# Kernel optimization log

Hardware: AMD Instinct MI355X
Metric: run time of the kernel (lower is better)

The kernel has to match this reference:

```python
import jax, jax.numpy as jnp
import numpy as np

RBF_CO = 10.077141124806595


def setup_inputs() -> dict:
    key = jax.random.key(0)
    k1, k2, k3 = jax.random.split(key, 3)
    n, dim = 2048, 128
    N, out_dim = 50000, 64
    features = jax.random.normal(k1, (n, dim), dtype=jnp.float32)
    train_data = jax.random.normal(k2, (N, dim), dtype=jnp.float32)
    weights = jax.random.normal(k3, (N, out_dim), dtype=jnp.float32) * 0.02
    return {"features": features, "train_data": train_data, "weights": weights}


def reference(features, train_data, weights):
    x2 = jnp.sum(features * features, axis=-1, keepdims=True)      # [n, 1]
    t2 = jnp.sum(train_data * train_data, axis=-1)                 # [N]
    d2 = x2 + t2[None, :] - 2.0 * (features @ train_data.T)        # [n, N]
    dist = jnp.sqrt(jnp.maximum(d2, 0.0))                          # clamp fp error
    k = jnp.exp(-dist / RBF_CO / 2.0)                              # RBF kernel [n, N]
    return k @ weights                                              # [n, out_dim]
```

## Files before the change

### kernel.cpp

```cpp
#include <hip/hip_runtime.h>
#include <hip/hip_bf16.h>
#include <stdint.h>

#define DIM 128
#define ODIM 64
#define BM 128
#define BN 64
#define NSPLIT 64

typedef __attribute__((ext_vector_type(8))) __bf16 bf16x8;
typedef __attribute__((ext_vector_type(4))) __bf16 bf16x4;
typedef __attribute__((ext_vector_type(2))) __bf16 bf16x2;
typedef __attribute__((ext_vector_type(4))) float f32x4;

#define MFMA_K32(a, b, c) __builtin_amdgcn_mfma_f32_16x16x32_bf16((a), (b), (c), 0, 0, 0)
#define MFMA_K16(a, b, c) __builtin_amdgcn_mfma_f32_16x16x16bf16_1k((a), (b), (c), 0, 0, 0)

#define RBFD 10.077141124806595
#define LOG2E 1.4426950408889634
#define C2D ((LOG2E / (2.0 * RBFD)) * (LOG2E / (2.0 * RBFD)))

__device__ __forceinline__ void async_copy16(const void* g, void* l) {
  __builtin_amdgcn_global_load_lds((const __attribute__((address_space(1))) void*)g,
                                   (__attribute__((address_space(3))) void*)l, 16, 0, 0);
}
__device__ __forceinline__ void async_copy4(const void* g, void* l) {
  __builtin_amdgcn_global_load_lds((const __attribute__((address_space(1))) void*)g,
                                   (__attribute__((address_space(3))) void*)l, 4, 0, 0);
}

__device__ __forceinline__ uint32_t pack_bf16(float a, float b) {
  uint32_t ua = __builtin_bit_cast(uint32_t, a) + 0x8000u;
  uint32_t ub = __builtin_bit_cast(uint32_t, b) + 0x8000u;
  return __builtin_amdgcn_perm(ub, ua, 0x07060302u);
}

__global__ void prep_all(const float* __restrict__ train, __bf16* __restrict__ Tb,
                         float* __restrict__ t2, const float* __restrict__ feat,
                         __bf16* __restrict__ Fb, float* __restrict__ x2,
                         const float* __restrict__ W, __bf16* __restrict__ Wt,
                         int Ntrain, int Npad, int nFeat, int tB, int fB, float scale) {
  __shared__ float tile[64][65];
  int b = blockIdx.x;
  int t = threadIdx.x;
  if (b < tB + fB) {
    const float* src;
    __bf16* dst;
    float* sq;
    int nValid, nPad, row0;
    float padv;
    if (b < tB) {
      src = train; dst = Tb; sq = t2; nValid = Ntrain; nPad = Npad; row0 = b * 4; padv = 1e30f;
    } else {
      src = feat; dst = Fb; sq = x2; nValid = nFeat; nPad = nFeat; row0 = (b - tB) * 4; padv = 0.0f;
    }
    int row = row0 + (t >> 6);
    int lane = t & 63;
    if (row >= nPad) return;
    float2 v = make_float2(0.0f, 0.0f);
    if (row < nValid) v = ((const float2*)src)[(size_t)row * 64 + lane];
    bf16x2 p;
    p.x = (__bf16)v.x;
    p.y = (__bf16)v.y;
    *(bf16x2*)&dst[(size_t)row * DIM + lane * 2] = p;
    float ss = v.x * v.x + v.y * v.y;
    #pragma unroll
    for (int off = 32; off > 0; off >>= 1) ss += __shfl_down(ss, off);
    if (lane == 0) sq[row] = (row < nValid) ? ss * scale : padv;
    return;
  }
  int j0 = (b - tB - fB) * 64;
  int jr = t >> 2;
  int cg = (t & 3) * 16;
  int j = j0 + jr;
  if (j < Ntrain) {
    const float4* src = (const float4*)(W + (size_t)j * ODIM);
    #pragma unroll
    for (int q = 0; q < 4; ++q) {
      float4 u = src[(cg >> 2) + q];
      tile[jr][cg + q * 4 + 0] = u.x;
      tile[jr][cg + q * 4 + 1] = u.y;
      tile[jr][cg + q * 4 + 2] = u.z;
      tile[jr][cg + q * 4 + 3] = u.w;
    }
  } else {
    #pragma unroll
    for (int q = 0; q < 16; ++q) tile[jr][cg + q] = 0.0f;
  }
  __syncthreads();
  int v = t >> 2;
  int jc = (t & 3) * 16;
  __bf16 ob[16];
  #pragma unroll
  for (int q = 0; q < 16; ++q) ob[q] = (__bf16)tile[jc + q][v];
  __bf16* dst = Wt + (size_t)v * Npad + j0 + jc;
  *(bf16x8*)dst = *(bf16x8*)&ob[0];
  *(bf16x8*)(dst + 8) = *(bf16x8*)&ob[8];
}

template <bool ATOMIC>
__global__ __launch_bounds__(256, 4) void rbf_main(
    const __bf16* __restrict__ Fb, const __bf16* __restrict__ Tb,
    const __bf16* __restrict__ Wt, const float* __restrict__ t2g,
    const float* __restrict__ x2g, float* __restrict__ outOrPart,
    int nRows, int Npad, int nChunks) {
  __shared__ __bf16 sT[BN * DIM];
  __shared__ __bf16 sW[ODIM * BN];
  __shared__ float st2[BN];

  const int tid = threadIdx.x;
  const int wave = tid >> 6;
  const int lane = tid & 63;
  const int l16 = lane & 15;
  const int g4 = lane >> 4;

  const int mb = (int)blockIdx.x;
  const int ns = (int)blockIdx.y;

  constexpr float KNEG2 = (float)(-2.0 * C2D);

  bf16x8 bF[2][4];
  #pragma unroll
  for (int nf = 0; nf < 2; ++nf)
    #pragma unroll
    for (int ko = 0; ko < 4; ++ko)
      bF[nf][ko] = *(const bf16x8*)(Fb + ((size_t)(mb * BM + wave * 32 + nf * 16 + l16)) * DIM +
                                    ko * 32 + g4 * 8);

  float x2v[2];
  #pragma unroll
  for (int nf = 0; nf < 2; ++nf)
    x2v[nf] = x2g[mb * BM + wave * 32 + nf * 16 + l16];

  f32x4 zero4 = {0.0f, 0.0f, 0.0f, 0.0f};
  f32x4 oacc[2][4];
  #pragma unroll
  for (int nf = 0; nf < 2; ++nf)
    #pragma unroll
    for (int vi = 0; vi < 4; ++vi) oacc[nf][vi] = zero4;

  for (int c = ns; c < nChunks; c += NSPLIT) {
    const int n0 = c * BN;

    {
      const char* gT = (const char*)Tb + (size_t)n0 * 256;
      #pragma unroll
      for (int i = 0; i < 4; ++i) {
        int off = i * 4096 + wave * 1024;
        int loff = off + lane * 16;
        int row = loff >> 8;
        int gran = (loff >> 4) & 15;
        async_copy16(gT + row * 256 + ((gran ^ (row & 15)) << 4), (char*)sT + off);
      }
    }
    {
      #pragma unroll
      for (int i = 0; i < 2; ++i) {
        int off = i * 4096 + wave * 1024;
        int loff = off + lane * 16;
        int v = loff >> 7;
        int gran = (loff >> 4) & 7;
        const char* gW = (const char*)Wt + ((size_t)v * Npad + n0) * 2 + ((gran ^ (v & 7)) << 4);
        async_copy16(gW, (char*)sW + off);
      }
    }
    if (wave == 0) async_copy4((const char*)(t2g + n0) + lane * 4, (char*)st2);
    __syncthreads();

    uint2 pk[4][2];
    #pragma unroll
    for (int mt = 0; mt < 4; ++mt) {
      f32x4 s0 = zero4, s1 = zero4;
      #pragma unroll
      for (int ko = 0; ko < 4; ++ko) {
        int slot = (ko * 4 + g4) ^ l16;
        bf16x8 a = *(const bf16x8*)((const char*)sT + (mt * 16 + l16) * 256 + (slot << 4));
        s0 = MFMA_K32(a, bF[0][ko], s0);
        s1 = MFMA_K32(a, bF[1][ko], s1);
      }
      f32x4 t2v = *(const f32x4*)&st2[mt * 16 + g4 * 4];
      float kv0[4], kv1[4];
      #pragma unroll
      for (int r = 0; r < 4; ++r) {
        float d20 = __builtin_fmaf(KNEG2, s0[r], t2v[r] + x2v[0]);
        float d21 = __builtin_fmaf(KNEG2, s1[r], t2v[r] + x2v[1]);
        kv0[r] = __builtin_amdgcn_exp2f(-__builtin_amdgcn_sqrtf(d20));
        kv1[r] = __builtin_amdgcn_exp2f(-__builtin_amdgcn_sqrtf(d21));
      }
      pk[mt][0] = make_uint2(pack_bf16(kv0[0], kv0[1]), pack_bf16(kv0[2], kv0[3]));
      pk[mt][1] = make_uint2(pack_bf16(kv1[0], kv1[1]), pack_bf16(kv1[2], kv1[3]));
    }

    #pragma unroll
    for (int vi = 0; vi < 4; ++vi) {
      int rowB = (vi * 16 + l16) * 128 + ((g4 & 1) << 3);
      #pragma unroll
      for (int mt = 0; mt < 4; ++mt) {
        int gran = (2 * mt + (g4 >> 1)) ^ (l16 & 7);
        bf16x4 wf = *(const bf16x4*)((const char*)sW + rowB + (gran << 4));
        oacc[0][vi] = MFMA_K16(__builtin_bit_cast(bf16x4, pk[mt][0]), wf, oacc[0][vi]);
        oacc[1][vi] = MFMA_K16(__builtin_bit_cast(bf16x4, pk[mt][1]), wf, oacc[1][vi]);
      }
    }
    __syncthreads();
  }

  if (ATOMIC) {
    float* out = outOrPart;
    #pragma unroll
    for (int nf = 0; nf < 2; ++nf)
      #pragma unroll
      for (int vi = 0; vi < 4; ++vi)
        #pragma unroll
        for (int r = 0; r < 4; ++r) {
          int row = mb * BM + wave * 32 + nf * 16 + g4 * 4 + r;
          int col = vi * 16 + l16;
          atomicAdd(&out[(size_t)row * ODIM + col], oacc[nf][vi][r]);
        }
  } else {
    float* dst = outOrPart + (size_t)ns * (size_t)nRows * ODIM;
    #pragma unroll
    for (int nf = 0; nf < 2; ++nf)
      #pragma unroll
      for (int vi = 0; vi < 4; ++vi)
        #pragma unroll
        for (int r = 0; r < 4; ++r) {
          int row = mb * BM + wave * 32 + nf * 16 + g4 * 4 + r;
          int col = vi * 16 + l16;
          dst[(size_t)row * ODIM + col] = oacc[nf][vi][r];
        }
  }
}

__global__ void reduce_parts(const float4* __restrict__ part, float4* __restrict__ out,
                             int total4) {
  int i = (int)blockIdx.x * blockDim.x + threadIdx.x;
  if (i >= total4) return;
  float4 s = make_float4(0.0f, 0.0f, 0.0f, 0.0f);
  #pragma unroll
  for (int sp = 0; sp < NSPLIT; ++sp) {
    float4 v = part[(size_t)sp * total4 + i];
    s.x += v.x; s.y += v.y; s.z += v.z; s.w += v.w;
  }
  out[i] = s;
}

extern "C" void kernel_launch(void* const* d_in, const int* in_sizes, int n_in,
                              void* d_out, int out_size, void* d_ws, size_t ws_size,
                              hipStream_t stream) {
  (void)n_in;
  const float* features = (const float*)d_in[0];
  const float* train = (const float*)d_in[1];
  const float* weights = (const float*)d_in[2];
  float* out = (float*)d_out;

  const int n = in_sizes[0] / DIM;
  const int N = in_sizes[1] / DIM;
  const int Npad = ((N + 63) / 64) * 64;
  const int nChunks = Npad / 64;

  size_t off = 0;
  auto alloc = [&](size_t bytes) {
    size_t o = off;
    off = (off + bytes + 255) & ~(size_t)255;
    return o;
  };
  size_t oT = alloc((size_t)Npad * DIM * 2);
  size_t oW = alloc((size_t)ODIM * Npad * 2);
  size_t oF = alloc((size_t)n * DIM * 2);
  size_t ot2 = alloc((size_t)Npad * 4);
  size_t ox2 = alloc((size_t)n * 4);
  size_t oPart = alloc((size_t)NSPLIT * n * ODIM * 4);
  size_t needFull = off;

  char* ws = (char*)d_ws;
  __bf16* Tb = (__bf16*)(ws + oT);
  __bf16* Wt = (__bf16*)(ws + oW);
  __bf16* Fb = (__bf16*)(ws + oF);
  float* t2 = (float*)(ws + ot2);
  float* x2 = (float*)(ws + ox2);

  const int tB = Npad / 4;
  const int fB = n / 4;
  const int wB = Npad / 64;
  prep_all<<<tB + fB + wB, 256, 0, stream>>>(train, Tb, t2, features, Fb, x2, weights, Wt,
                                             N, Npad, n, tB, fB, (float)C2D);

  const int mBlocks = n / BM;
  dim3 grid(mBlocks, NSPLIT);

  if (ws_size >= needFull) {
    float* part = (float*)(ws + oPart);
    rbf_main<false><<<grid, 256, 0, stream>>>(Fb, Tb, Wt, t2, x2, part, n, Npad, nChunks);
    int total4 = n * ODIM / 4;
    reduce_parts<<<(total4 + 255) / 256, 256, 0, stream>>>((const float4*)part, (float4*)out,
                                                           total4);
  } else {
    hipMemsetAsync(d_out, 0, (size_t)out_size * sizeof(float), stream);
    rbf_main<true><<<grid, 256, 0, stream>>>(Fb, Tb, Wt, t2, x2, out, n, Npad, nChunks);
  }
}
```

Before: 146.5 us.

## Raise split-N count, swap grid axes, precompute LDS and global offsets

Splits the N dimension 96 ways instead of 64, with a 32-way fallback when the workspace is small. The grid is reordered so the split index is the fast axis, which groups blocks sharing a train chunk or a feature block together. Launch bounds rise to 6 blocks per SM. Per-iteration address arithmetic for the swizzled LDS reads and the async global copies is hoisted into precomputed offsets and pointer increments. Together these aim at better occupancy and less integer overhead per chunk, at the cost of more partial-buffer traffic in the reduction and tighter register limits.

```diff
diff --git a/kernel.cpp b/kernel.cpp
--- a/kernel.cpp
+++ b/kernel.cpp
@@ -6,7 +6,6 @@
 #define ODIM 64
 #define BM 128
 #define BN 64
-#define NSPLIT 64
 
 typedef __attribute__((ext_vector_type(8))) __bf16 bf16x8;
 typedef __attribute__((ext_vector_type(4))) __bf16 bf16x4;
@@ -98,8 +97,8 @@
   *(bf16x8*)(dst + 8) = *(bf16x8*)&ob[8];
 }
 
-template <bool ATOMIC>
-__global__ __launch_bounds__(256, 4) void rbf_main(
+template <int NS, bool ATOMIC>
+__global__ __launch_bounds__(256, 6) void rbf_main(
     const __bf16* __restrict__ Fb, const __bf16* __restrict__ Tb,
     const __bf16* __restrict__ Wt, const float* __restrict__ t2g,
     const float* __restrict__ x2g, float* __restrict__ outOrPart,
@@ -114,10 +113,45 @@
   const int l16 = lane & 15;
   const int g4 = lane >> 4;
 
-  const int mb = (int)blockIdx.x;
-  const int ns = (int)blockIdx.y;
+  const int ns = (int)blockIdx.x;
+  const int mb = (int)blockIdx.y;
 
   constexpr float KNEG2 = (float)(-2.0 * C2D);
+
+  int aOff[4];
+  #pragma unroll
+  for (int ko = 0; ko < 4; ++ko) aOff[ko] = l16 * 256 + (((ko * 4 + g4) ^ l16) << 4);
+  int wOff[4];
+  #pragma unroll
+  for (int mt = 0; mt < 4; ++mt)
+    wOff[mt] = l16 * 128 + ((g4 & 1) << 3) + ((((2 * mt + (g4 >> 1)) ^ (l16 & 7))) << 4);
+
+  int tGOff[4], ldsOffT[4];
+  #pragma unroll
+  for (int i = 0; i < 4; ++i) {
+    int off = i * 4096 + wave * 1024;
+    int loff = off + lane * 16;
+    int row = loff >> 8;
+    int gran = (loff >> 4) & 15;
+    ldsOffT[i] = off;
+    tGOff[i] = row * 256 + ((gran ^ (row & 15)) << 4);
+  }
+  int wGOff[2], ldsOffW[2];
+  #pragma unroll
+  for (int i = 0; i < 2; ++i) {
+    int off = i * 4096 + wave * 1024;
+    int loff = off + lane * 16;
+    int v = loff >> 7;
+    int gran = (loff >> 4) & 7;
+    ldsOffW[i] = off;
+    wGOff[i] = v * (Npad * 2) + ((gran ^ (v & 7)) << 4);
+  }
+  const char* gTbase = (const char*)Tb + (size_t)ns * (BN * 256);
+  const char* gWbase = (const char*)Wt + (size_t)ns * (BN * 2);
+  const char* gt2 = (const char*)(t2g) + (size_t)ns * (BN * 4) + lane * 4;
+  const size_t strT = (size_t)NS * (BN * 256);
+  const size_t strW = (size_t)NS * (BN * 2);
+  const size_t str2 = (size_t)NS * (BN * 4);
 
   bf16x8 bF[2][4];
   #pragma unroll
@@ -126,7 +160,6 @@
     for (int ko = 0; ko < 4; ++ko)
       bF[nf][ko] = *(const bf16x8*)(Fb + ((size_t)(mb * BM + wave * 32 + nf * 16 + l16)) * DIM +
                                     ko * 32 + g4 * 8);
-
   float x2v[2];
   #pragma unroll
   for (int nf = 0; nf < 2; ++nf)
@@ -139,32 +172,15 @@
     #pragma unroll
     for (int vi = 0; vi < 4; ++vi) oacc[nf][vi] = zero4;
 
-  for (int c = ns; c < nChunks; c += NSPLIT) {
-    const int n0 = c * BN;
-
-    {
-      const char* gT = (const char*)Tb + (size_t)n0 * 256;
-      #pragma unroll
-      for (int i = 0; i < 4; ++i) {
-        int off = i * 4096 + wave * 1024;
-        int loff = off + lane * 16;
-        int row = loff >> 8;
-        int gran = (loff >> 4) & 15;
-        async_copy16(gT + row * 256 + ((gran ^ (row & 15)) << 4), (char*)sT + off);
-      }
-    }
-    {
-      #pragma unroll
-      for (int i = 0; i < 2; ++i) {
-        int off = i * 4096 + wave * 1024;
-        int loff = off + lane * 16;
-        int v = loff >> 7;
-        int gran = (loff >> 4) & 7;
-        const char* gW = (const char*)Wt + ((size_t)v * Npad + n0) * 2 + ((gran ^ (v & 7)) << 4);
-        async_copy16(gW, (char*)sW + off);
-      }
-    }
-    if (wave == 0) async_copy4((const char*)(t2g + n0) + lane * 4, (char*)st2);
+  for (int c = ns; c < nChunks; c += NS) {
+    #pragma unroll
+    for (int i = 0; i < 4; ++i) async_copy16(gTbase + tGOff[i], (char*)sT + ldsOffT[i]);
+    #pragma unroll
+    for (int i = 0; i < 2; ++i) async_copy16(gWbase + wGOff[i], (char*)sW + ldsOffW[i]);
+    if (wave == 0) async_copy4(gt2, (char*)st2);
+    gTbase += strT;
+    gWbase += strW;
+    gt2 += str2;
     __syncthreads();
 
     uint2 pk[4][2];
@@ -173,8 +189,7 @@
       f32x4 s0 = zero4, s1 = zero4;
       #pragma unroll
       for (int ko = 0; ko < 4; ++ko) {
-        int slot = (ko * 4 + g4) ^ l16;
-        bf16x8 a = *(const bf16x8*)((const char*)sT + (mt * 16 + l16) * 256 + (slot << 4));
+        bf16x8 a = *(const bf16x8*)((const char*)sT + aOff[ko] + mt * 4096);
         s0 = MFMA_K32(a, bF[0][ko], s0);
         s1 = MFMA_K32(a, bF[1][ko], s1);
       }
@@ -193,11 +208,9 @@
 
     #pragma unroll
     for (int vi = 0; vi < 4; ++vi) {
-      int rowB = (vi * 16 + l16) * 128 + ((g4 & 1) << 3);
       #pragma unroll
       for (int mt = 0; mt < 4; ++mt) {
-        int gran = (2 * mt + (g4 >> 1)) ^ (l16 & 7);
-        bf16x4 wf = *(const bf16x4*)((const char*)sW + rowB + (gran << 4));
+        bf16x4 wf = *(const bf16x4*)((const char*)sW + wOff[mt] + vi * 2048);
         oacc[0][vi] = MFMA_K16(__builtin_bit_cast(bf16x4, pk[mt][0]), wf, oacc[0][vi]);
         oacc[1][vi] = MFMA_K16(__builtin_bit_cast(bf16x4, pk[mt][1]), wf, oacc[1][vi]);
       }
@@ -232,13 +245,14 @@
   }
 }
 
+template <int NS>
 __global__ void reduce_parts(const float4* __restrict__ part, float4* __restrict__ out,
                              int total4) {
   int i = (int)blockIdx.x * blockDim.x + threadIdx.x;
   if (i >= total4) return;
   float4 s = make_float4(0.0f, 0.0f, 0.0f, 0.0f);
   #pragma unroll
-  for (int sp = 0; sp < NSPLIT; ++sp) {
+  for (int sp = 0; sp < NS; ++sp) {
     float4 v = part[(size_t)sp * total4 + i];
     s.x += v.x; s.y += v.y; s.z += v.z; s.w += v.w;
   }
@@ -270,8 +284,8 @@
   size_t oF = alloc((size_t)n * DIM * 2);
   size_t ot2 = alloc((size_t)Npad * 4);
   size_t ox2 = alloc((size_t)n * 4);
-  size_t oPart = alloc((size_t)NSPLIT * n * ODIM * 4);
-  size_t needFull = off;
+  size_t bufEnd = off;
+  size_t oPart = alloc(0);
 
   char* ws = (char*)d_ws;
   __bf16* Tb = (__bf16*)(ws + oT);
@@ -279,6 +293,7 @@
   __bf16* Fb = (__bf16*)(ws + oF);
   float* t2 = (float*)(ws + ot2);
   float* x2 = (float*)(ws + ox2);
+  float* part = (float*)(ws + oPart);
 
   const int tB = Npad / 4;
   const int fB = n / 4;
@@ -287,16 +302,22 @@
                                              N, Npad, n, tB, fB, (float)C2D);
 
   const int mBlocks = n / BM;
-  dim3 grid(mBlocks, NSPLIT);
-
-  if (ws_size >= needFull) {
-    float* part = (float*)(ws + oPart);
-    rbf_main<false><<<grid, 256, 0, stream>>>(Fb, Tb, Wt, t2, x2, part, n, Npad, nChunks);
-    int total4 = n * ODIM / 4;
-    reduce_parts<<<(total4 + 255) / 256, 256, 0, stream>>>((const float4*)part, (float4*)out,
-                                                           total4);
+  const int total4 = n * ODIM / 4;
+  const size_t partBytes = (size_t)n * ODIM * 4;
+
+  if (ws_size >= bufEnd + 96 * partBytes) {
+    rbf_main<96, false><<<dim3(96, mBlocks), 256, 0, stream>>>(Fb, Tb, Wt, t2, x2, part, n,
+                                                               Npad, nChunks);
+    reduce_parts<96><<<(total4 + 255) / 256, 256, 0, stream>>>((const float4*)part,
+                                                               (float4*)out, total4);
+  } else if (ws_size >= bufEnd + 32 * partBytes) {
+    rbf_main<32, false><<<dim3(32, mBlocks), 256, 0, stream>>>(Fb, Tb, Wt, t2, x2, part, n,
+                                                               Npad, nChunks);
+    reduce_parts<32><<<(total4 + 255) / 256, 256, 0, stream>>>((const float4*)part,
+                                                               (float4*)out, total4);
   } else {
     hipMemsetAsync(d_out, 0, (size_t)out_size * sizeof(float), stream);
-    rbf_main<true><<<grid, 256, 0, stream>>>(Fb, Tb, Wt, t2, x2, out, n, Npad, nChunks);
-  }
-}
+    rbf_main<96, true><<<dim3(96, mBlocks), 256, 0, stream>>>(Fb, Tb, Wt, t2, x2, out, n,
+                                                              Npad, nChunks);
+  }
+}
```

After: 395.7 us. 2.7x slower.
